# Kernel optimization log

Hardware: AMD Instinct MI355X
Metric: run time of the kernel (lower is better)

## Reference

```python
import jax, jax.numpy as jnp
import numpy as np
from jax import lax

VOCAB_SIZE = 13
E = 13          # embedding_dim == len(VOCAB)
H = 1024        # weights_dim (LSTM hidden)
HL = 512        # hidden_layer_dim (MLP)
OUT = 2
T = 16384       # sequence length


def setup_inputs() -> dict:
    key = jax.random.key(0)
    ks = jax.random.split(key, 12)
    s_ih = 1.0 / np.sqrt(H)  # PyTorch LSTMCell default init scale
    inp = {
        "x": jax.random.normal(ks[0], (T, E), dtype=jnp.float32),
        "h0": jax.random.normal(ks[1], (1, H), dtype=jnp.float32) * np.sqrt(2.0 / (1 + H)),
        "c0": jax.random.normal(ks[2], (1, H), dtype=jnp.float32) * np.sqrt(2.0 / (1 + H)),
        "W_ih": jax.random.uniform(ks[3], (4 * H, E), jnp.float32, -s_ih, s_ih),
        "W_hh": jax.random.uniform(ks[4], (4 * H, H), jnp.float32, -s_ih, s_ih),
        "b_ih": jax.random.uniform(ks[5], (4 * H,), jnp.float32, -s_ih, s_ih),
        "b_hh": jax.random.uniform(ks[6], (4 * H,), jnp.float32, -s_ih, s_ih),
        "W1": jax.random.uniform(ks[7], (HL, H), jnp.float32, -1.0 / np.sqrt(H), 1.0 / np.sqrt(H)),
        "b1": jax.random.uniform(ks[8], (HL,), jnp.float32, -1.0 / np.sqrt(H), 1.0 / np.sqrt(H)),
        "W2": jax.random.uniform(ks[9], (OUT, HL), jnp.float32, -1.0 / np.sqrt(HL), 1.0 / np.sqrt(HL)),
        "b2": jax.random.uniform(ks[10], (OUT,), jnp.float32, -1.0 / np.sqrt(HL), 1.0 / np.sqrt(HL)),
    }
    return inp


def reference(x, h0, c0, W_ih, W_hh, b_ih, b_hh, W1, b1, W2, b2):
    # x: [T, E] (batch dim of the original view is 1, folded away)
    # Precompute input-to-gate projections for all timesteps (same math, one GEMM).
    xg = x @ W_ih.T + b_ih  # [T, 4H]

    def step(carry, xg_t):
        h, c = carry  # [1, H] each
        gates = xg_t + h @ W_hh.T + b_hh  # [1, 4H]
        i, f, g, o = jnp.split(gates, 4, axis=-1)
        c = jax.nn.sigmoid(f) * c + jax.nn.sigmoid(i) * jnp.tanh(g)
        h = jax.nn.sigmoid(o) * jnp.tanh(c)
        return (h, c), None

    (h, c), _ = lax.scan(step, (h0, c0), xg[:, None, :])
    out = jnp.tanh(h @ W1.T + b1) @ W2.T + b2  # [1, 2]
    return out
```

## Files before the change

### kernel.cpp

```cpp
#include <hip/hip_runtime.h>
#include <cstdint>
#include <cstddef>

#define NWG 64
#define NTHR 512
#define TSTEPS 16384
#define HDIM 1024
#define EDIM 13
#define HLDIM 512

typedef unsigned long long ull;

__global__ void k_init(const float* __restrict__ h0, ull* __restrict__ hrec,
                       ull* __restrict__ urec) {
  int i = threadIdx.x;
  hrec[i] = (ull)__float_as_uint(h0[i]);
  hrec[HDIM + i] = 0ull;
  hrec[2 * HDIM + i] = 0ull;
  hrec[3 * HDIM + i] = 0ull;
  if (i < HLDIM) urec[i] = 0ull;
}

__global__ __launch_bounds__(NTHR, 2) void k_main(
    const float* __restrict__ x, const float* __restrict__ c0,
    const float* __restrict__ Wih, const float* __restrict__ Whh,
    const float* __restrict__ bih, const float* __restrict__ bhh,
    const float* __restrict__ W1, const float* __restrict__ b1,
    const float* __restrict__ W2, const float* __restrict__ b2,
    float* __restrict__ out, ull* hrec, ull* urec) {
  const int w = blockIdx.x;
  const int tid = threadIdx.x;
  const int sub = tid & 7;
  const int row = tid >> 3;
  const int wave = tid >> 6;
  const int lane = tid & 63;
  const int g = row & 3;
  const int lu = row >> 2;
  const int grow = g * HDIM + w * 16 + lu;

  __shared__ float4 lds_h4[2][HDIM / 4];
  __shared__ float lds_x[2][16];
  __shared__ float lds_wih[64][17];
  __shared__ float lds_bsum[64];
  __shared__ float lds_r0[8], lds_r1[8];
  float* lds_hf = (float*)lds_h4;

  float4 wreg[32];
  const float4* wrow = (const float4*)(Whh + (size_t)grow * HDIM) + sub * 32;
#pragma unroll
  for (int i = 0; i < 32; ++i) wreg[i] = wrow[(i + sub) & 31];
#pragma unroll
  for (int i = 0; i < 32; ++i)
    asm volatile("" : "+v"(wreg[i].x), "+v"(wreg[i].y), "+v"(wreg[i].z),
                     "+v"(wreg[i].w));

  if (tid < 64) {
    int g2 = tid & 3, lu2 = tid >> 2;
    int gr2 = g2 * HDIM + w * 16 + lu2;
#pragma unroll
    for (int e = 0; e < EDIM; ++e) lds_wih[tid][e] = Wih[gr2 * EDIM + e];
    lds_bsum[tid] = bih[gr2] + bhh[gr2];
  }
  float cst = c0[w * 16 + 2 * wave + (lane >> 5)];
  __syncthreads();

  const float gsc = (g == 2) ? 2.f : 1.f;

  for (int t = 1; t <= TSTEPS; ++t) {
    const int lp = (t - 1) & 1;
    float xv = 0.f;
    if (tid < EDIM) xv = x[(size_t)(t - 1) * EDIM + tid];

    const ull* src = hrec + (size_t)((t - 1) & 3) * HDIM;
    const unsigned want = (unsigned)(t - 1);
    ull v0 = __hip_atomic_load(&src[tid], __ATOMIC_RELAXED,
                               __HIP_MEMORY_SCOPE_AGENT);
    ull v1 = __hip_atomic_load(&src[tid + NTHR], __ATOMIC_RELAXED,
                               __HIP_MEMORY_SCOPE_AGENT);
    for (;;) {
      bool b0 = (unsigned)(v0 >> 32) == want;
      bool b1 = (unsigned)(v1 >> 32) == want;
      if (b0 && b1) break;
      if (!b0)
        v0 = __hip_atomic_load(&src[tid], __ATOMIC_RELAXED,
                               __HIP_MEMORY_SCOPE_AGENT);
      if (!b1)
        v1 = __hip_atomic_load(&src[tid + NTHR], __ATOMIC_RELAXED,
                               __HIP_MEMORY_SCOPE_AGENT);
    }
    lds_hf[lp * HDIM + tid] = __uint_as_float((unsigned)v0);
    lds_hf[lp * HDIM + tid + NTHR] = __uint_as_float((unsigned)v1);
    if (tid < EDIM) lds_x[lp][tid] = xv;
    __syncthreads();

    float acc = lds_wih[row][sub] * lds_x[lp][sub];
    if (sub < EDIM - 8) acc += lds_wih[row][sub + 8] * lds_x[lp][sub + 8];
    if (sub == 0) acc += lds_bsum[row];
#pragma unroll
    for (int i = 0; i < 32; ++i) {
      float4 hv = lds_h4[lp][sub * 32 + ((i + sub) & 31)];
      float4 wv = wreg[i];
      acc += wv.x * hv.x;
      acc += wv.y * hv.y;
      acc += wv.z * hv.z;
      acc += wv.w * hv.w;
    }
    acc += __shfl_xor(acc, 1);
    acc += __shfl_xor(acc, 2);
    acc += __shfl_xor(acc, 4);

    float e = __expf(-gsc * acc);
    float y = 1.f / (1.f + e);
    float act = (g == 2) ? 2.f * y - 1.f : y;

    int base = lane & 32;
    float ai = __shfl(act, base + 0);
    float af = __shfl(act, base + 8);
    float ag = __shfl(act, base + 16);
    float ao = __shfl(act, base + 24);
    if ((lane & 31) == 0) {
      cst = af * cst + ai * ag;
      float e2 = __expf(-2.f * cst);
      float hn = ao * (2.f / (1.f + e2) - 1.f);
      ull pk = ((ull)(unsigned)t << 32) | (ull)__float_as_uint(hn);
      __hip_atomic_store(&hrec[(size_t)(t & 3) * HDIM + w * 16 + 2 * wave +
                               (lane >> 5)],
                         pk, __ATOMIC_RELAXED, __HIP_MEMORY_SCOPE_AGENT);
    }
  }

  {
    const unsigned want = (unsigned)TSTEPS;
    ull v0 = __hip_atomic_load(&hrec[tid], __ATOMIC_RELAXED,
                               __HIP_MEMORY_SCOPE_AGENT);
    ull v1 = __hip_atomic_load(&hrec[tid + NTHR], __ATOMIC_RELAXED,
                               __HIP_MEMORY_SCOPE_AGENT);
    for (;;) {
      bool b0 = (unsigned)(v0 >> 32) == want;
      bool b1 = (unsigned)(v1 >> 32) == want;
      if (b0 && b1) break;
      if (!b0)
        v0 = __hip_atomic_load(&hrec[tid], __ATOMIC_RELAXED,
                               __HIP_MEMORY_SCOPE_AGENT);
      if (!b1)
        v1 = __hip_atomic_load(&hrec[tid + NTHR], __ATOMIC_RELAXED,
                               __HIP_MEMORY_SCOPE_AGENT);
    }
    lds_hf[tid] = __uint_as_float((unsigned)v0);
    lds_hf[tid + NTHR] = __uint_as_float((unsigned)v1);
  }
  __syncthreads();
  {
    int r1 = 8 * w + wave;
    const float* w1p = W1 + (size_t)r1 * HDIM + lane * 16;
    float acc1 = 0.f;
#pragma unroll
    for (int i = 0; i < 16; ++i) acc1 += w1p[i] * lds_hf[lane * 16 + i];
#pragma unroll
    for (int m = 1; m < 64; m <<= 1) acc1 += __shfl_xor(acc1, m);
    if (lane == 0) {
      float e2 = __expf(-2.f * (acc1 + b1[r1]));
      float u = 2.f / (1.f + e2) - 1.f;
      ull pk = (1ull << 32) | (ull)__float_as_uint(u);
      __hip_atomic_store(&urec[r1], pk, __ATOMIC_RELAXED,
                         __HIP_MEMORY_SCOPE_AGENT);
    }
  }

  if (w == 0) {
    ull uv = __hip_atomic_load(&urec[tid], __ATOMIC_RELAXED,
                               __HIP_MEMORY_SCOPE_AGENT);
    while ((unsigned)(uv >> 32) != 1u)
      uv = __hip_atomic_load(&urec[tid], __ATOMIC_RELAXED,
                             __HIP_MEMORY_SCOPE_AGENT);
    float u = __uint_as_float((unsigned)uv);
    float p0 = W2[tid] * u;
    float p1 = W2[HLDIM + tid] * u;
#pragma unroll
    for (int m = 1; m < 64; m <<= 1) {
      p0 += __shfl_xor(p0, m);
      p1 += __shfl_xor(p1, m);
    }
    if (lane == 0) {
      lds_r0[wave] = p0;
      lds_r1[wave] = p1;
    }
    __syncthreads();
    if (tid == 0) {
      float o0 = b2[0], o1 = b2[1];
#pragma unroll
      for (int k = 0; k < 8; ++k) {
        o0 += lds_r0[k];
        o1 += lds_r1[k];
      }
      out[0] = o0;
      out[1] = o1;
    }
  }
}

extern "C" void kernel_launch(void* const* d_in, const int* in_sizes, int n_in,
                              void* d_out, int out_size, void* d_ws,
                              size_t ws_size, hipStream_t stream) {
  const float* x = (const float*)d_in[0];
  const float* h0 = (const float*)d_in[1];
  const float* c0 = (const float*)d_in[2];
  const float* Wih = (const float*)d_in[3];
  const float* Whh = (const float*)d_in[4];
  const float* bih = (const float*)d_in[5];
  const float* bhh = (const float*)d_in[6];
  const float* W1 = (const float*)d_in[7];
  const float* b1 = (const float*)d_in[8];
  const float* W2 = (const float*)d_in[9];
  const float* b2 = (const float*)d_in[10];
  float* out = (float*)d_out;

  ull* hrec = (ull*)d_ws;
  ull* urec = (ull*)((char*)d_ws + 4 * HDIM * sizeof(ull));

  k_init<<<1, 1024, 0, stream>>>(h0, hrec, urec);
  k_main<<<NWG, NTHR, 0, stream>>>(x, c0, Wih, Whh, bih, bhh, W1, b1, W2, b2,
                                   out, hrec, urec);
}
```

Baseline: 51.62 ms.

## Spread LSTM recurrence over 128 workgroups with LDS-resident weights and per-wave units

Doubles the workgroup count to 128 so each handles 8 hidden units instead of 16. The recurrent weight slice (32 rows × 1024) moves from registers into LDS, about 128KB per block. Each wave now computes the four gates of one hidden unit with a full 64-lane reduction, and s_sleep is added to the spin-wait loops. The aim is to cut per-step matvec latency, at the cost of more workgroups taking part in the global per-step barrier and LDS-bandwidth-bound reads instead of register-resident weights.

```diff
diff --git a/kernel.cpp b/kernel.cpp
--- a/kernel.cpp
+++ b/kernel.cpp
@@ -2,8 +2,9 @@
 #include <cstdint>
 #include <cstddef>
 
-#define NWG 64
+#define NWG 128
 #define NTHR 512
+#define UPW 8
 #define TSTEPS 16384
 #define HDIM 1024
 #define EDIM 13
@@ -21,7 +22,7 @@
   if (i < HLDIM) urec[i] = 0ull;
 }
 
-__global__ __launch_bounds__(NTHR, 2) void k_main(
+__global__ __launch_bounds__(NTHR) void k_main(
     const float* __restrict__ x, const float* __restrict__ c0,
     const float* __restrict__ Wih, const float* __restrict__ Whh,
     const float* __restrict__ bih, const float* __restrict__ bhh,
@@ -30,41 +31,39 @@
     float* __restrict__ out, ull* hrec, ull* urec) {
   const int w = blockIdx.x;
   const int tid = threadIdx.x;
-  const int sub = tid & 7;
-  const int row = tid >> 3;
   const int wave = tid >> 6;
   const int lane = tid & 63;
-  const int g = row & 3;
-  const int lu = row >> 2;
-  const int grow = g * HDIM + w * 16 + lu;
-
-  __shared__ float4 lds_h4[2][HDIM / 4];
+
+  __shared__ float4 lds_w4[32 * 256];
+  __shared__ float4 lds_h4[2 * 256];
   __shared__ float lds_x[2][16];
-  __shared__ float lds_wih[64][17];
-  __shared__ float lds_bsum[64];
+  __shared__ float lds_wih[32][17];
+  __shared__ float lds_bsum[32];
   __shared__ float lds_r0[8], lds_r1[8];
-  float* lds_hf = (float*)lds_h4;
-
-  float4 wreg[32];
-  const float4* wrow = (const float4*)(Whh + (size_t)grow * HDIM) + sub * 32;
-#pragma unroll
-  for (int i = 0; i < 32; ++i) wreg[i] = wrow[(i + sub) & 31];
-#pragma unroll
-  for (int i = 0; i < 32; ++i)
-    asm volatile("" : "+v"(wreg[i].x), "+v"(wreg[i].y), "+v"(wreg[i].z),
-                     "+v"(wreg[i].w));
-
-  if (tid < 64) {
-    int g2 = tid & 3, lu2 = tid >> 2;
-    int gr2 = g2 * HDIM + w * 16 + lu2;
-#pragma unroll
-    for (int e = 0; e < EDIM; ++e) lds_wih[tid][e] = Wih[gr2 * EDIM + e];
-    lds_bsum[tid] = bih[gr2] + bhh[gr2];
-  }
-  float cst = c0[w * 16 + 2 * wave + (lane >> 5)];
+
+#pragma unroll
+  for (int it = 0; it < 16; ++it) {
+    int idx = it * NTHR + tid;
+    int r = idx >> 8;
+    int c4 = idx & 255;
+    int v0_ = r >> 2, g0_ = r & 3;
+    int grow = g0_ * HDIM + UPW * w + v0_;
+    lds_w4[r * 256 + c4] =
+        ((const float4*)(Whh + (size_t)grow * HDIM))[c4];
+  }
+  if (tid < 32) {
+    int v0_ = tid >> 2, g0_ = tid & 3;
+    int grow = g0_ * HDIM + UPW * w + v0_;
+#pragma unroll
+    for (int e = 0; e < EDIM; ++e) lds_wih[tid][e] = Wih[grow * EDIM + e];
+    lds_bsum[tid] = bih[grow] + bhh[grow];
+  }
+  float cst = c0[UPW * w + wave];
   __syncthreads();
 
-  const float gsc = (g == 2) ? 2.f : 1.f;
+  const int myg = lane & 3;
+  const float gsc = (myg == 2) ? 2.f : 1.f;
+  const float4* wb = lds_w4 + (wave * 4) * 256;
 
   for (int t = 1; t <= TSTEPS; ++t) {
     const int lp = (t - 1) & 1;
@@ -73,96 +72,151 @@
 
     const ull* src = hrec + (size_t)((t - 1) & 3) * HDIM;
     const unsigned want = (unsigned)(t - 1);
-    ull v0 = __hip_atomic_load(&src[tid], __ATOMIC_RELAXED,
-                               __HIP_MEMORY_SCOPE_AGENT);
-    ull v1 = __hip_atomic_load(&src[tid + NTHR], __ATOMIC_RELAXED,
+    ull r0 = __hip_atomic_load(&src[2 * tid], __ATOMIC_RELAXED,
+                               __HIP_MEMORY_SCOPE_AGENT);
+    ull r1 = __hip_atomic_load(&src[2 * tid + 1], __ATOMIC_RELAXED,
                                __HIP_MEMORY_SCOPE_AGENT);
     for (;;) {
-      bool b0 = (unsigned)(v0 >> 32) == want;
-      bool b1 = (unsigned)(v1 >> 32) == want;
+      bool b0 = (unsigned)(r0 >> 32) == want;
+      bool b1 = (unsigned)(r1 >> 32) == want;
       if (b0 && b1) break;
+      __builtin_amdgcn_s_sleep(2);
       if (!b0)
-        v0 = __hip_atomic_load(&src[tid], __ATOMIC_RELAXED,
+        r0 = __hip_atomic_load(&src[2 * tid], __ATOMIC_RELAXED,
                                __HIP_MEMORY_SCOPE_AGENT);
       if (!b1)
-        v1 = __hip_atomic_load(&src[tid + NTHR], __ATOMIC_RELAXED,
-                               __HIP_MEMORY_SCOPE_AGENT);
-    }
-    lds_hf[lp * HDIM + tid] = __uint_as_float((unsigned)v0);
-    lds_hf[lp * HDIM + tid + NTHR] = __uint_as_float((unsigned)v1);
+        r1 = __hip_atomic_load(&src[2 * tid + 1], __ATOMIC_RELAXED,
+                               __HIP_MEMORY_SCOPE_AGENT);
+    }
+    float2 hv;
+    hv.x = __uint_as_float((unsigned)r0);
+    hv.y = __uint_as_float((unsigned)r1);
+    ((float2*)lds_h4)[lp * 512 + tid] = hv;
     if (tid < EDIM) lds_x[lp][tid] = xv;
     __syncthreads();
 
-    float acc = lds_wih[row][sub] * lds_x[lp][sub];
-    if (sub < EDIM - 8) acc += lds_wih[row][sub + 8] * lds_x[lp][sub + 8];
-    if (sub == 0) acc += lds_bsum[row];
-#pragma unroll
-    for (int i = 0; i < 32; ++i) {
-      float4 hv = lds_h4[lp][sub * 32 + ((i + sub) & 31)];
-      float4 wv = wreg[i];
-      acc += wv.x * hv.x;
-      acc += wv.y * hv.y;
-      acc += wv.z * hv.z;
-      acc += wv.w * hv.w;
-    }
-    acc += __shfl_xor(acc, 1);
-    acc += __shfl_xor(acc, 2);
-    acc += __shfl_xor(acc, 4);
-
-    float e = __expf(-gsc * acc);
+    const float4* hb = lds_h4 + lp * 256;
+    float4 h0 = hb[lane], h1 = hb[lane + 64], h2 = hb[lane + 128],
+           h3 = hb[lane + 192];
+
+    float acc0, acc1, acc2, acc3;
+    {
+      float4 a = wb[lane], b = wb[lane + 64], c = wb[lane + 128],
+             d = wb[lane + 192];
+      acc0 = (a.x * h0.x + a.y * h0.y + a.z * h0.z + a.w * h0.w) +
+             (b.x * h1.x + b.y * h1.y + b.z * h1.z + b.w * h1.w) +
+             (c.x * h2.x + c.y * h2.y + c.z * h2.z + c.w * h2.w) +
+             (d.x * h3.x + d.y * h3.y + d.z * h3.z + d.w * h3.w);
+    }
+    {
+      const float4* wr = wb + 256;
+      float4 a = wr[lane], b = wr[lane + 64], c = wr[lane + 128],
+             d = wr[lane + 192];
+      acc1 = (a.x * h0.x + a.y * h0.y + a.z * h0.z + a.w * h0.w) +
+             (b.x * h1.x + b.y * h1.y + b.z * h1.z + b.w * h1.w) +
+             (c.x * h2.x + c.y * h2.y + c.z * h2.z + c.w * h2.w) +
+             (d.x * h3.x + d.y * h3.y + d.z * h3.z + d.w * h3.w);
+    }
+    {
+      const float4* wr = wb + 512;
+      float4 a = wr[lane], b = wr[lane + 64], c = wr[lane + 128],
+             d = wr[lane + 192];
+      acc2 = (a.x * h0.x + a.y * h0.y + a.z * h0.z + a.w * h0.w) +
+             (b.x * h1.x + b.y * h1.y + b.z * h1.z + b.w * h1.w) +
+             (c.x * h2.x + c.y * h2.y + c.z * h2.z + c.w * h2.w) +
+             (d.x * h3.x + d.y * h3.y + d.z * h3.z + d.w * h3.w);
+    }
+    {
+      const float4* wr = wb + 768;
+      float4 a = wr[lane], b = wr[lane + 64], c = wr[lane + 128],
+             d = wr[lane + 192];
+      acc3 = (a.x * h0.x + a.y * h0.y + a.z * h0.z + a.w * h0.w) +
+             (b.x * h1.x + b.y * h1.y + b.z * h1.z + b.w * h1.w) +
+             (c.x * h2.x + c.y * h2.y + c.z * h2.z + c.w * h2.w) +
+             (d.x * h3.x + d.y * h3.y + d.z * h3.z + d.w * h3.w);
+    }
+
+    if (lane < 4) {
+      int lrow = wave * 4 + lane;
+      float xd = lds_bsum[lrow];
+#pragma unroll
+      for (int e = 0; e < EDIM; ++e) xd += lds_wih[lrow][e] * lds_x[lp][e];
+      if (lane == 0) acc0 += xd;
+      else if (lane == 1) acc1 += xd;
+      else if (lane == 2) acc2 += xd;
+      else acc3 += xd;
+    }
+
+#pragma unroll
+    for (int m = 1; m < 64; m <<= 1) {
+      acc0 += __shfl_xor(acc0, m);
+      acc1 += __shfl_xor(acc1, m);
+      acc2 += __shfl_xor(acc2, m);
+      acc3 += __shfl_xor(acc3, m);
+    }
+
+    float pre = (myg == 0) ? acc0 : (myg == 1) ? acc1 : (myg == 2) ? acc2
+                                                                   : acc3;
+    float e = __expf(-gsc * pre);
     float y = 1.f / (1.f + e);
-    float act = (g == 2) ? 2.f * y - 1.f : y;
-
-    int base = lane & 32;
-    float ai = __shfl(act, base + 0);
-    float af = __shfl(act, base + 8);
-    float ag = __shfl(act, base + 16);
-    float ao = __shfl(act, base + 24);
-    if ((lane & 31) == 0) {
+    float act = (myg == 2) ? 2.f * y - 1.f : y;
+
+    float ai = __shfl(act, 0);
+    float af = __shfl(act, 1);
+    float ag = __shfl(act, 2);
+    float ao = __shfl(act, 3);
+    if (lane == 0) {
       cst = af * cst + ai * ag;
       float e2 = __expf(-2.f * cst);
       float hn = ao * (2.f / (1.f + e2) - 1.f);
       ull pk = ((ull)(unsigned)t << 32) | (ull)__float_as_uint(hn);
-      __hip_atomic_store(&hrec[(size_t)(t & 3) * HDIM + w * 16 + 2 * wave +
-                               (lane >> 5)],
-                         pk, __ATOMIC_RELAXED, __HIP_MEMORY_SCOPE_AGENT);
+      __hip_atomic_store(&hrec[(size_t)(t & 3) * HDIM + UPW * w + wave], pk,
+                         __ATOMIC_RELAXED, __HIP_MEMORY_SCOPE_AGENT);
     }
   }
 
   {
     const unsigned want = (unsigned)TSTEPS;
-    ull v0 = __hip_atomic_load(&hrec[tid], __ATOMIC_RELAXED,
-                               __HIP_MEMORY_SCOPE_AGENT);
-    ull v1 = __hip_atomic_load(&hrec[tid + NTHR], __ATOMIC_RELAXED,
+    ull r0 = __hip_atomic_load(&hrec[2 * tid], __ATOMIC_RELAXED,
+                               __HIP_MEMORY_SCOPE_AGENT);
+    ull r1 = __hip_atomic_load(&hrec[2 * tid + 1], __ATOMIC_RELAXED,
                                __HIP_MEMORY_SCOPE_AGENT);
     for (;;) {
-      bool b0 = (unsigned)(v0 >> 32) == want;
-      bool b1 = (unsigned)(v1 >> 32) == want;
+      bool b0 = (unsigned)(r0 >> 32) == want;
+      bool b1 = (unsigned)(r1 >> 32) == want;
       if (b0 && b1) break;
+      __builtin_amdgcn_s_sleep(2);
       if (!b0)
-        v0 = __hip_atomic_load(&hrec[tid], __ATOMIC_RELAXED,
+        r0 = __hip_atomic_load(&hrec[2 * tid], __ATOMIC_RELAXED,
                                __HIP_MEMORY_SCOPE_AGENT);
       if (!b1)
-        v1 = __hip_atomic_load(&hrec[tid + NTHR], __ATOMIC_RELAXED,
-                               __HIP_MEMORY_SCOPE_AGENT);
-    }
-    lds_hf[tid] = __uint_as_float((unsigned)v0);
-    lds_hf[tid + NTHR] = __uint_as_float((unsigned)v1);
+        r1 = __hip_atomic_load(&hrec[2 * tid + 1], __ATOMIC_RELAXED,
+                               __HIP_MEMORY_SCOPE_AGENT);
+    }
+    float2 hv;
+    hv.x = __uint_as_float((unsigned)r0);
+    hv.y = __uint_as_float((unsigned)r1);
+    ((float2*)lds_h4)[tid] = hv;
   }
   __syncthreads();
-  {
-    int r1 = 8 * w + wave;
-    const float* w1p = W1 + (size_t)r1 * HDIM + lane * 16;
-    float acc1 = 0.f;
-#pragma unroll
-    for (int i = 0; i < 16; ++i) acc1 += w1p[i] * lds_hf[lane * 16 + i];
+  if (wave < 4) {
+    int r1i = 4 * w + wave;
+    const float* hf = (const float*)lds_h4;
+    const float* w1p = W1 + (size_t)r1i * HDIM + lane * 16;
+    float a0 = 0.f, a1 = 0.f;
+#pragma unroll
+    for (int i = 0; i < 16; i += 2) {
+      a0 += w1p[i] * hf[lane * 16 + i];
+      a1 += w1p[i + 1] * hf[lane * 16 + i + 1];
+    }
+    float acc1 = a0 + a1;
 #pragma unroll
     for (int m = 1; m < 64; m <<= 1) acc1 += __shfl_xor(acc1, m);
     if (lane == 0) {
-      float e2 = __expf(-2.f * (acc1 + b1[r1]));
+      float e2 = __expf(-2.f * (acc1 + b1[r1i]));
       float u = 2.f / (1.f + e2) - 1.f;
       ull pk = (1ull << 32) | (ull)__float_as_uint(u);
-      __hip_atomic_store(&urec[r1], pk, __ATOMIC_RELAXED,
+      __hip_atomic_store(&urec[r1i], pk, __ATOMIC_RELAXED,
                          __HIP_MEMORY_SCOPE_AGENT);
     }
   }
@@ -170,9 +224,11 @@
   if (w == 0) {
     ull uv = __hip_atomic_load(&urec[tid], __ATOMIC_RELAXED,
                                __HIP_MEMORY_SCOPE_AGENT);
-    while ((unsigned)(uv >> 32) != 1u)
+    while ((unsigned)(uv >> 32) != 1u) {
+      __builtin_amdgcn_s_sleep(2);
       uv = __hip_atomic_load(&urec[tid], __ATOMIC_RELAXED,
                              __HIP_MEMORY_SCOPE_AGENT);
+    }
     float u = __uint_as_float((unsigned)uv);
     float p0 = W2[tid] * u;
     float p1 = W2[HLDIM + tid] * u;
```

After: 75.99 ms. 1.47x slower.

## Move W_hh slice from registers to LDS/global with per-unit row dot products

Applied to the files above, without the earlier changes.

Each workgroup no longer keeps its W_hh slice in registers (8 lanes per gate row). Each half-wave now computes one hidden unit's four gate rows across 32 lanes. Half the units read weights from a 128KB LDS copy, and the other half stream them from global memory every timestep. The aim is to relieve register pressure and change the reduction shape, but the global half must re-read 64KB per workgroup per step through the cache on the serial critical path, so latency may rise. Minor tweaks: split accumulators in the MLP dot and an extra barrier before the final reduction.

```diff
diff --git a/kernel.cpp b/kernel.cpp
--- a/kernel.cpp
+++ b/kernel.cpp
@@ -4,6 +4,7 @@
 
 #define NWG 64
 #define NTHR 512
+#define UPW 16
 #define TSTEPS 16384
 #define HDIM 1024
 #define EDIM 13
@@ -21,7 +22,7 @@
   if (i < HLDIM) urec[i] = 0ull;
 }
 
-__global__ __launch_bounds__(NTHR, 2) void k_main(
+__global__ __launch_bounds__(NTHR) void k_main(
     const float* __restrict__ x, const float* __restrict__ c0,
     const float* __restrict__ Wih, const float* __restrict__ Whh,
     const float* __restrict__ bih, const float* __restrict__ bhh,
@@ -30,41 +31,54 @@
     float* __restrict__ out, ull* hrec, ull* urec) {
   const int w = blockIdx.x;
   const int tid = threadIdx.x;
-  const int sub = tid & 7;
-  const int row = tid >> 3;
   const int wave = tid >> 6;
   const int lane = tid & 63;
-  const int g = row & 3;
-  const int lu = row >> 2;
-  const int grow = g * HDIM + w * 16 + lu;
-
-  __shared__ float4 lds_h4[2][HDIM / 4];
-  __shared__ float lds_x[2][16];
+  const int hi = lane >> 5;
+  const int sl = lane & 31;
+  const int lu = 2 * wave + hi;
+
+  __shared__ float4 lds_w4[32 * 256];
+  __shared__ float4 lds_h4[2 * 256];
   __shared__ float lds_wih[64][17];
   __shared__ float lds_bsum[64];
   __shared__ float lds_r0[8], lds_r1[8];
   float* lds_hf = (float*)lds_h4;
-
-  float4 wreg[32];
-  const float4* wrow = (const float4*)(Whh + (size_t)grow * HDIM) + sub * 32;
-#pragma unroll
-  for (int i = 0; i < 32; ++i) wreg[i] = wrow[(i + sub) & 31];
-#pragma unroll
-  for (int i = 0; i < 32; ++i)
-    asm volatile("" : "+v"(wreg[i].x), "+v"(wreg[i].y), "+v"(wreg[i].z),
-                     "+v"(wreg[i].w));
-
+  float* lds_x0 = (float*)lds_r0;
+  __shared__ float lds_xbuf[2][16];
+
+#pragma unroll
+  for (int it = 0; it < 16; ++it) {
+    int idx = it * NTHR + tid;
+    int r = idx >> 8;
+    int c4 = idx & 255;
+    int lu_ = r >> 2, g_ = r & 3;
+    int grow = g_ * HDIM + UPW * w + lu_;
+    lds_w4[r * 256 + c4] = ((const float4*)(Whh + (size_t)grow * HDIM))[c4];
+  }
   if (tid < 64) {
-    int g2 = tid & 3, lu2 = tid >> 2;
-    int gr2 = g2 * HDIM + w * 16 + lu2;
-#pragma unroll
-    for (int e = 0; e < EDIM; ++e) lds_wih[tid][e] = Wih[gr2 * EDIM + e];
-    lds_bsum[tid] = bih[gr2] + bhh[gr2];
-  }
-  float cst = c0[w * 16 + 2 * wave + (lane >> 5)];
+    int lu_ = tid >> 2, g_ = tid & 3;
+    int grow = g_ * HDIM + UPW * w + lu_;
+#pragma unroll
+    for (int e = 0; e < EDIM; ++e) lds_wih[tid][e] = Wih[grow * EDIM + e];
+    lds_bsum[tid] = bih[grow] + bhh[grow];
+  }
+  float cst = c0[UPW * w + lu];
   __syncthreads();
 
-  const float gsc = (g == 2) ? 2.f : 1.f;
+  const int myg = sl & 3;
+  const float gsc = (myg == 2) ? 2.f : 1.f;
+  const float4* wl0 = lds_w4 + (size_t)(4 * lu + 0) * 256;
+  const float4* wl1 = lds_w4 + (size_t)(4 * lu + 1) * 256;
+  const float4* wl2 = lds_w4 + (size_t)(4 * lu + 2) * 256;
+  const float4* wl3 = lds_w4 + (size_t)(4 * lu + 3) * 256;
+  const float4* gg0 =
+      (const float4*)(Whh + (size_t)(0 * HDIM + UPW * w + lu) * HDIM);
+  const float4* gg1 =
+      (const float4*)(Whh + (size_t)(1 * HDIM + UPW * w + lu) * HDIM);
+  const float4* gg2 =
+      (const float4*)(Whh + (size_t)(2 * HDIM + UPW * w + lu) * HDIM);
+  const float4* gg3 =
+      (const float4*)(Whh + (size_t)(3 * HDIM + UPW * w + lu) * HDIM);
 
   for (int t = 1; t <= TSTEPS; ++t) {
     const int lp = (t - 1) & 1;
@@ -90,42 +104,81 @@
     }
     lds_hf[lp * HDIM + tid] = __uint_as_float((unsigned)v0);
     lds_hf[lp * HDIM + tid + NTHR] = __uint_as_float((unsigned)v1);
-    if (tid < EDIM) lds_x[lp][tid] = xv;
+    if (tid < EDIM) lds_xbuf[lp][tid] = xv;
     __syncthreads();
 
-    float acc = lds_wih[row][sub] * lds_x[lp][sub];
-    if (sub < EDIM - 8) acc += lds_wih[row][sub + 8] * lds_x[lp][sub + 8];
-    if (sub == 0) acc += lds_bsum[row];
-#pragma unroll
-    for (int i = 0; i < 32; ++i) {
-      float4 hv = lds_h4[lp][sub * 32 + ((i + sub) & 31)];
-      float4 wv = wreg[i];
-      acc += wv.x * hv.x;
-      acc += wv.y * hv.y;
-      acc += wv.z * hv.z;
-      acc += wv.w * hv.w;
-    }
-    acc += __shfl_xor(acc, 1);
-    acc += __shfl_xor(acc, 2);
-    acc += __shfl_xor(acc, 4);
-
-    float e = __expf(-gsc * acc);
+    const float4* hb = lds_h4 + lp * 256;
+    float4 hv0 = hb[sl], hv1 = hb[sl + 32], hv2 = hb[sl + 64],
+           hv3 = hb[sl + 96], hv4 = hb[sl + 128], hv5 = hb[sl + 160],
+           hv6 = hb[sl + 192], hv7 = hb[sl + 224];
+
+#define ROWDOT(dst, srcp)                                                 \
+  {                                                                       \
+    float4 a = (srcp)[sl], b = (srcp)[sl + 32], c = (srcp)[sl + 64],      \
+           d = (srcp)[sl + 96], e4 = (srcp)[sl + 128],                    \
+           f4 = (srcp)[sl + 160], g4 = (srcp)[sl + 192],                  \
+           i4 = (srcp)[sl + 224];                                         \
+    dst = (a.x * hv0.x + a.y * hv0.y + a.z * hv0.z + a.w * hv0.w) +       \
+          (b.x * hv1.x + b.y * hv1.y + b.z * hv1.z + b.w * hv1.w) +       \
+          (c.x * hv2.x + c.y * hv2.y + c.z * hv2.z + c.w * hv2.w) +       \
+          (d.x * hv3.x + d.y * hv3.y + d.z * hv3.z + d.w * hv3.w) +       \
+          (e4.x * hv4.x + e4.y * hv4.y + e4.z * hv4.z + e4.w * hv4.w) +   \
+          (f4.x * hv5.x + f4.y * hv5.y + f4.z * hv5.z + f4.w * hv5.w) +   \
+          (g4.x * hv6.x + g4.y * hv6.y + g4.z * hv6.z + g4.w * hv6.w) +   \
+          (i4.x * hv7.x + i4.y * hv7.y + i4.z * hv7.z + i4.w * hv7.w);    \
+  }
+
+    float acc0, acc1, acc2, acc3;
+    if (lu < 8) {
+      ROWDOT(acc0, wl0);
+      ROWDOT(acc1, wl1);
+      ROWDOT(acc2, wl2);
+      ROWDOT(acc3, wl3);
+    } else {
+      ROWDOT(acc0, gg0);
+      ROWDOT(acc1, gg1);
+      ROWDOT(acc2, gg2);
+      ROWDOT(acc3, gg3);
+    }
+#undef ROWDOT
+
+    if (sl < 4) {
+      int lrow = lu * 4 + sl;
+      float xd = lds_bsum[lrow];
+#pragma unroll
+      for (int e = 0; e < EDIM; ++e) xd += lds_wih[lrow][e] * lds_xbuf[lp][e];
+      if (sl == 0) acc0 += xd;
+      else if (sl == 1) acc1 += xd;
+      else if (sl == 2) acc2 += xd;
+      else acc3 += xd;
+    }
+
+#pragma unroll
+    for (int m = 1; m < 32; m <<= 1) {
+      acc0 += __shfl_xor(acc0, m);
+      acc1 += __shfl_xor(acc1, m);
+      acc2 += __shfl_xor(acc2, m);
+      acc3 += __shfl_xor(acc3, m);
+    }
+
+    float pre = (myg == 0) ? acc0 : (myg == 1) ? acc1 : (myg == 2) ? acc2
+                                                                   : acc3;
+    float e = __expf(-gsc * pre);
     float y = 1.f / (1.f + e);
-    float act = (g == 2) ? 2.f * y - 1.f : y;
+    float act = (myg == 2) ? 2.f * y - 1.f : y;
 
     int base = lane & 32;
     float ai = __shfl(act, base + 0);
-    float af = __shfl(act, base + 8);
-    float ag = __shfl(act, base + 16);
-    float ao = __shfl(act, base + 24);
-    if ((lane & 31) == 0) {
+    float af = __shfl(act, base + 1);
+    float ag = __shfl(act, base + 2);
+    float ao = __shfl(act, base + 3);
+    if (sl == 0) {
       cst = af * cst + ai * ag;
       float e2 = __expf(-2.f * cst);
       float hn = ao * (2.f / (1.f + e2) - 1.f);
       ull pk = ((ull)(unsigned)t << 32) | (ull)__float_as_uint(hn);
-      __hip_atomic_store(&hrec[(size_t)(t & 3) * HDIM + w * 16 + 2 * wave +
-                               (lane >> 5)],
-                         pk, __ATOMIC_RELAXED, __HIP_MEMORY_SCOPE_AGENT);
+      __hip_atomic_store(&hrec[(size_t)(t & 3) * HDIM + UPW * w + lu], pk,
+                         __ATOMIC_RELAXED, __HIP_MEMORY_SCOPE_AGENT);
     }
   }
 
@@ -153,9 +206,13 @@
   {
     int r1 = 8 * w + wave;
     const float* w1p = W1 + (size_t)r1 * HDIM + lane * 16;
-    float acc1 = 0.f;
-#pragma unroll
-    for (int i = 0; i < 16; ++i) acc1 += w1p[i] * lds_hf[lane * 16 + i];
+    float a0 = 0.f, a1 = 0.f;
+#pragma unroll
+    for (int i = 0; i < 16; i += 2) {
+      a0 += w1p[i] * lds_hf[lane * 16 + i];
+      a1 += w1p[i + 1] * lds_hf[lane * 16 + i + 1];
+    }
+    float acc1 = a0 + a1;
 #pragma unroll
     for (int m = 1; m < 64; m <<= 1) acc1 += __shfl_xor(acc1, m);
     if (lane == 0) {
@@ -181,6 +238,7 @@
       p0 += __shfl_xor(p0, m);
       p1 += __shfl_xor(p1, m);
     }
+    __syncthreads();
     if (lane == 0) {
       lds_r0[wave] = p0;
       lds_r1[wave] = p1;
```

New measurement: 59.55 ms. 1.15x slower.

## Halve workgroup count, doubling hidden units and register-resident weights per block

Applied to the files above, without the earlier changes.

Shrinks the persistent grid from 64 to 32 workgroups, so each block owns 32 hidden units and each thread holds 64 float4 of W_hh in registers (4 threads per gate row instead of 8). This cuts the number of blocks polling the global h records each step and shortens the cross-lane reduction. The dot products use four independent accumulators to break the FMA dependency chain. The cost is twice as many FMAs per thread per step and about 256 VGPRs of weights per thread, which risks spilling and lower occupancy.

```diff
diff --git a/kernel.cpp b/kernel.cpp
--- a/kernel.cpp
+++ b/kernel.cpp
@@ -2,8 +2,9 @@
 #include <cstdint>
 #include <cstddef>
 
-#define NWG 64
+#define NWG 32
 #define NTHR 512
+#define UPW 32
 #define TSTEPS 16384
 #define HDIM 1024
 #define EDIM 13
@@ -21,7 +22,7 @@
   if (i < HLDIM) urec[i] = 0ull;
 }
 
-__global__ __launch_bounds__(NTHR, 2) void k_main(
+__global__ __launch_bounds__(NTHR) void k_main(
     const float* __restrict__ x, const float* __restrict__ c0,
     const float* __restrict__ Wih, const float* __restrict__ Whh,
     const float* __restrict__ bih, const float* __restrict__ bhh,
@@ -30,38 +31,38 @@
     float* __restrict__ out, ull* hrec, ull* urec) {
   const int w = blockIdx.x;
   const int tid = threadIdx.x;
-  const int sub = tid & 7;
-  const int row = tid >> 3;
+  const int sub4 = tid & 3;
+  const int row = tid >> 2;
   const int wave = tid >> 6;
   const int lane = tid & 63;
   const int g = row & 3;
   const int lu = row >> 2;
-  const int grow = g * HDIM + w * 16 + lu;
+  const int grow = g * HDIM + w * UPW + lu;
 
   __shared__ float4 lds_h4[2][HDIM / 4];
   __shared__ float lds_x[2][16];
-  __shared__ float lds_wih[64][17];
-  __shared__ float lds_bsum[64];
+  __shared__ float lds_wih[128][17];
+  __shared__ float lds_bsum[128];
   __shared__ float lds_r0[8], lds_r1[8];
   float* lds_hf = (float*)lds_h4;
 
-  float4 wreg[32];
-  const float4* wrow = (const float4*)(Whh + (size_t)grow * HDIM) + sub * 32;
-#pragma unroll
-  for (int i = 0; i < 32; ++i) wreg[i] = wrow[(i + sub) & 31];
-#pragma unroll
-  for (int i = 0; i < 32; ++i)
+  float4 wreg[64];
+  const float4* wrow = (const float4*)(Whh + (size_t)grow * HDIM) + sub4 * 64;
+#pragma unroll
+  for (int i = 0; i < 64; ++i) wreg[i] = wrow[(i + sub4) & 63];
+#pragma unroll
+  for (int i = 0; i < 64; ++i)
     asm volatile("" : "+v"(wreg[i].x), "+v"(wreg[i].y), "+v"(wreg[i].z),
                      "+v"(wreg[i].w));
 
-  if (tid < 64) {
+  if (tid < 128) {
     int g2 = tid & 3, lu2 = tid >> 2;
-    int gr2 = g2 * HDIM + w * 16 + lu2;
+    int gr2 = g2 * HDIM + w * UPW + lu2;
 #pragma unroll
     for (int e = 0; e < EDIM; ++e) lds_wih[tid][e] = Wih[gr2 * EDIM + e];
     lds_bsum[tid] = bih[gr2] + bhh[gr2];
   }
-  float cst = c0[w * 16 + 2 * wave + (lane >> 5)];
+  float cst = c0[w * UPW + 4 * wave + (lane >> 4)];
   __syncthreads();
 
   const float gsc = (g == 2) ? 2.f : 1.f;
@@ -93,38 +94,42 @@
     if (tid < EDIM) lds_x[lp][tid] = xv;
     __syncthreads();
 
-    float acc = lds_wih[row][sub] * lds_x[lp][sub];
-    if (sub < EDIM - 8) acc += lds_wih[row][sub + 8] * lds_x[lp][sub + 8];
-    if (sub == 0) acc += lds_bsum[row];
-#pragma unroll
-    for (int i = 0; i < 32; ++i) {
-      float4 hv = lds_h4[lp][sub * 32 + ((i + sub) & 31)];
+    float a0 = 0.f, a1 = 0.f, a2 = 0.f, a3 = 0.f;
+    if (sub4 == 0) {
+      a0 = lds_bsum[row];
+#pragma unroll
+      for (int e = 0; e < EDIM; ++e) a0 += lds_wih[row][e] * lds_x[lp][e];
+    }
+#pragma unroll
+    for (int i = 0; i < 64; ++i) {
+      float4 hv = lds_h4[lp][sub4 * 64 + ((i + sub4) & 63)];
       float4 wv = wreg[i];
-      acc += wv.x * hv.x;
-      acc += wv.y * hv.y;
-      acc += wv.z * hv.z;
-      acc += wv.w * hv.w;
-    }
+      float p = wv.x * hv.x + wv.y * hv.y + wv.z * hv.z + wv.w * hv.w;
+      if ((i & 3) == 0) a0 += p;
+      else if ((i & 3) == 1) a1 += p;
+      else if ((i & 3) == 2) a2 += p;
+      else a3 += p;
+    }
+    float acc = (a0 + a1) + (a2 + a3);
     acc += __shfl_xor(acc, 1);
     acc += __shfl_xor(acc, 2);
-    acc += __shfl_xor(acc, 4);
 
     float e = __expf(-gsc * acc);
     float y = 1.f / (1.f + e);
     float act = (g == 2) ? 2.f * y - 1.f : y;
 
-    int base = lane & 32;
+    int base = lane & 48;
     float ai = __shfl(act, base + 0);
-    float af = __shfl(act, base + 8);
-    float ag = __shfl(act, base + 16);
-    float ao = __shfl(act, base + 24);
-    if ((lane & 31) == 0) {
+    float af = __shfl(act, base + 4);
+    float ag = __shfl(act, base + 8);
+    float ao = __shfl(act, base + 12);
+    if ((lane & 15) == 0) {
       cst = af * cst + ai * ag;
       float e2 = __expf(-2.f * cst);
       float hn = ao * (2.f / (1.f + e2) - 1.f);
       ull pk = ((ull)(unsigned)t << 32) | (ull)__float_as_uint(hn);
-      __hip_atomic_store(&hrec[(size_t)(t & 3) * HDIM + w * 16 + 2 * wave +
-                               (lane >> 5)],
+      __hip_atomic_store(&hrec[(size_t)(t & 3) * HDIM + w * UPW + 4 * wave +
+                               (lane >> 4)],
                          pk, __ATOMIC_RELAXED, __HIP_MEMORY_SCOPE_AGENT);
     }
   }
@@ -150,12 +155,17 @@
     lds_hf[tid + NTHR] = __uint_as_float((unsigned)v1);
   }
   __syncthreads();
-  {
-    int r1 = 8 * w + wave;
+#pragma unroll
+  for (int half = 0; half < 2; ++half) {
+    int r1 = 16 * w + 8 * half + wave;
     const float* w1p = W1 + (size_t)r1 * HDIM + lane * 16;
-    float acc1 = 0.f;
-#pragma unroll
-    for (int i = 0; i < 16; ++i) acc1 += w1p[i] * lds_hf[lane * 16 + i];
+    float s0 = 0.f, s1 = 0.f;
+#pragma unroll
+    for (int i = 0; i < 16; i += 2) {
+      s0 += w1p[i] * lds_hf[lane * 16 + i];
+      s1 += w1p[i + 1] * lds_hf[lane * 16 + i + 1];
+    }
+    float acc1 = s0 + s1;
 #pragma unroll
     for (int m = 1; m < 64; m <<= 1) acc1 += __shfl_xor(acc1, m);
     if (lane == 0) {
```

Result: slower. 142.1 ms (+175.4%).
